# Performance work log

Hardware: AMD Instinct MI355X
Metric: run time of the kernel (lower is better)

Reference implementation:

```python
import jax, jax.numpy as jnp
import numpy as np

N = 262144
HID = 200


def _lin_init(k, out_d, in_d):
    k1, k2 = jax.random.split(k)
    bound = 1.0 / np.sqrt(in_d)
    W = jax.random.uniform(k1, (out_d, in_d), minval=-bound, maxval=bound, dtype=jnp.float32)
    b = jax.random.uniform(k2, (out_d,), minval=-bound, maxval=bound, dtype=jnp.float32)
    return W, b


def setup_inputs() -> dict:
    key = jax.random.key(0)
    ks = jax.random.split(key, 10)
    Wu0, bu0 = _lin_init(ks[0], HID, 3)
    Wu1, bu1 = _lin_init(ks[1], HID, HID)
    Wu2, bu2 = _lin_init(ks[2], 1, HID)
    Wv0, bv0 = _lin_init(ks[3], HID, 3)
    Wv1, bv1 = _lin_init(ks[4], HID, HID)
    Wv2, bv2 = _lin_init(ks[5], 1, HID)
    Wf0, bf0 = _lin_init(ks[6], HID, 12)
    Wf1, bf1 = _lin_init(ks[7], HID, HID)
    Wf2, bf2 = _lin_init(ks[8], 2, HID)
    inputs = jax.random.normal(ks[9], (N, 3), dtype=jnp.float32)
    return dict(inputs=inputs,
                Wu0=Wu0, bu0=bu0, Wu1=Wu1, bu1=bu1, Wu2=Wu2, bu2=bu2,
                Wv0=Wv0, bv0=bv0, Wv1=Wv1, bv1=bv1, Wv2=Wv2, bv2=bv2,
                Wf0=Wf0, bf0=bf0, Wf1=Wf1, bf1=bf1, Wf2=Wf2, bf2=bf2)


def _mlp(x, W0, b0, W1, b1, W2, b2):
    # NN with num_layers=3: sin(Linear) -> sin(Linear) -> Linear
    h = jnp.sin(x @ W0.T + b0)
    h = jnp.sin(h @ W1.T + b1)
    return h @ W2.T + b2


def _scalar(pt, params):
    # per-point scalar network, pt: [3]
    W0, b0, W1, b1, W2, b2 = params
    h = jnp.sin(W0 @ pt + b0)
    h = jnp.sin(W1 @ h + b1)
    return (W2 @ h + b2)[0]


def _derivs(pt, params):
    # first derivatives (grad) and diagonal second derivatives u_xx, u_yy
    # via forward-over-reverse (jvp of grad) with unit tangents e_x, e_y.
    g = jax.grad(lambda p: _scalar(p, params))
    ex = jnp.array([1.0, 0.0, 0.0], dtype=pt.dtype)
    ey = jnp.array([0.0, 1.0, 0.0], dtype=pt.dtype)
    grad, hx = jax.jvp(g, (pt,), (ex,))
    _, hy = jax.jvp(g, (pt,), (ey,))
    return grad, hx[0], hy[1]


def _dhpm_forward(inputs, pu, pv, pf):
    u = _mlp(inputs, *pu)  # [N,1]
    v = _mlp(inputs, *pv)  # [N,1]
    gu, u_xx, u_yy = jax.vmap(lambda p: _derivs(p, pu))(inputs)
    gv, v_xx, v_yy = jax.vmap(lambda p: _derivs(p, pv))(inputs)
    u_x, u_y, u_t = gu[:, :1], gu[:, 1:2], gu[:, 2:3]
    v_x, v_y, v_t = gv[:, :1], gv[:, 1:2], gv[:, 2:3]
    u_xx = u_xx[:, None]; u_yy = u_yy[:, None]
    v_xx = v_xx[:, None]; v_yy = v_yy[:, None]
    feat = jnp.concatenate([u, v, u_t, v_t, u_x, u_xx, u_y, u_yy,
                            v_x, v_xx, v_y, v_yy], axis=1)  # [N,12]
    f = _mlp(feat, *pf)  # [N,2]
    return (u, v, u_t, v_t, u_x, u_xx, u_y, u_yy,
            v_x, v_xx, v_y, v_yy, f[:, :1], f[:, 1:])


def reference(inputs, Wu0, bu0, Wu1, bu1, Wu2, bu2,
              Wv0, bv0, Wv1, bv1, Wv2, bv2,
              Wf0, bf0, Wf1, bf1, Wf2, bf2):
    pu = (Wu0, bu0, Wu1, bu1, Wu2, bu2)
    pv = (Wv0, bv0, Wv1, bv1, Wv2, bv2)
    pf = (Wf0, bf0, Wf1, bf1, Wf2, bf2)
    return _dhpm_forward(inputs, pu, pv, pf)
```

## Files before the change

kernel.cpp:

```cpp
#include <hip/hip_runtime.h>


#define HID 200
#define NPTS 128
#define NTHREADS 512
#define NT 13
#define KT 7
#define BLDK 232
#define BCHUNK 45056
#define FCHUNK 8192
#define XLDP 132

#define OFF_U  0
#define OFF_V  585728
#define OFF_F  1171456
#define OFF_CU 1277952
#define OFF_CV 1281152
#define OFF_CF 1284352

typedef _Float16 f16;
typedef _Float16 f16x2 __attribute__((ext_vector_type(2)));
typedef _Float16 f16x8 __attribute__((ext_vector_type(8)));
typedef float f32x4 __attribute__((ext_vector_type(4)));

#define GLDS16(gp, lp) __builtin_amdgcn_global_load_lds( \
    (const __attribute__((address_space(1))) void*)(gp), \
    (__attribute__((address_space(3))) void*)(lp), 16, 0, 0)

__global__ __launch_bounds__(256) void dhpm_prep(
    const float* __restrict__ Wu0, const float* __restrict__ bu0, const float* __restrict__ Wu1,
    const float* __restrict__ Wv0, const float* __restrict__ bv0, const float* __restrict__ Wv1,
    const float* __restrict__ Wf0, const float* __restrict__ bf0, const float* __restrict__ Wf1,
    char* __restrict__ ws)
{
    const int id = blockIdx.x * blockDim.x + threadIdx.x;
    const int nB = 2 * NT * 96 * 116;
    const int nF = NT * 16 * 116;
    if (id < nB) {
        int e = id;
        const int net = e / (NT*96*116); e -= net * (NT*96*116);
        const int nt  = e / (96*116);    e -= nt * (96*116);
        const int row = e / 116;
        const int k2  = e - row*116;
        const int ch  = row >> 4;
        const int j   = nt*16 + (row & 15);
        const int k   = k2*2;
        const float* W0 = net ? Wv0 : Wu0;
        const float* W1 = net ? Wv1 : Wu1;
        f16x2 v; v[0] = (f16)0.f; v[1] = (f16)0.f;
        if (j < HID) {
            #pragma unroll
            for (int s = 0; s < 2; ++s) {
                const int ks = k + s;
                if (ks < HID) {
                    const float w1 = W1[j*HID + ks];
                    const float ax = W0[ks*3+0], ay = W0[ks*3+1], at = W0[ks*3+2];
                    float gg;
                    if      (ch == 0) gg = 1.f;
                    else if (ch == 1) gg = -ax*ax;
                    else if (ch == 2) gg = -ay*ay;
                    else if (ch == 3) gg = ax;
                    else if (ch == 4) gg = ay;
                    else              gg = at;
                    v[s] = (f16)(w1 * gg);
                }
            }
        }
        *(f16x2*)(ws + (net ? OFF_V : OFF_U) + nt*BCHUNK + row*464 + k2*4) = v;
        return;
    }
    if (id < nB + nF) {
        int e = id - nB;
        const int nt  = e / (16*116);  e -= nt * (16*116);
        const int row = e / 116;
        const int k2  = e - row*116;
        const int j   = nt*16 + row;
        const int k   = k2*2;
        f16x2 v; v[0] = (f16)0.f; v[1] = (f16)0.f;
        if (j < HID) {
            if (k     < HID) v[0] = (f16)Wf1[j*HID + k];
            if (k + 1 < HID) v[1] = (f16)Wf1[j*HID + k + 1];
        }
        *(f16x2*)(ws + OFF_F + nt*FCHUNK + row*464 + k2*4) = v;
        return;
    }
    if (id < nB + nF + 400) {
        const int e = id - nB - nF;
        const int net = e / HID;
        const int r   = e - net*HID;
        const float* W0 = net ? Wv0 : Wu0;
        const float* b0 = net ? bv0 : bu0;
        float4 c;
        c.x = W0[r*3+0]; c.y = W0[r*3+1]; c.z = W0[r*3+2]; c.w = b0[r];
        *(float4*)(ws + (net ? OFF_CV : OFF_CU) + r*16) = c;
        return;
    }
    if (id < nB + nF + 400 + HID) {
        const int i = id - nB - nF - 400;
        float4 c0, c1, c2, c3;
        c0.x = Wf0[i*12+0];  c0.y = Wf0[i*12+1];  c0.z = Wf0[i*12+2];  c0.w = Wf0[i*12+3];
        c1.x = Wf0[i*12+4];  c1.y = Wf0[i*12+5];  c1.z = Wf0[i*12+6];  c1.w = Wf0[i*12+7];
        c2.x = Wf0[i*12+8];  c2.y = Wf0[i*12+9];  c2.z = Wf0[i*12+10]; c2.w = Wf0[i*12+11];
        c3.x = bf0[i]; c3.y = 0.f; c3.z = 0.f; c3.w = 0.f;
        char* p = ws + OFF_CF + i*64;
        *(float4*)(p)      = c0;
        *(float4*)(p + 16) = c1;
        *(float4*)(p + 32) = c2;
        *(float4*)(p + 48) = c3;
    }
}

__device__ __forceinline__ void run_net(
    const float* __restrict__ inp, const char* __restrict__ ws,
    const int cstOff, const int bOff,
    const float* __restrict__ b1, const float* __restrict__ W2, const float b2s,
    const int colV, const int colX, const int colXX,
    const int colY, const int colYY, const int colT,
    char* __restrict__ Bst, float* __restrict__ exch, float* __restrict__ featL,
    float* __restrict__ out, const int Np, const int gp0)
{
    const int t = threadIdx.x;
    const int lane = t & 63;
    const int w = __builtin_amdgcn_readfirstlane(t >> 6);
    const int q = w & 3, g = w >> 2;
    const int jl = lane & 15, klo = lane >> 4;

    const char* bsrc = ws + bOff;

    for (int c = w; c < 44; c += 8)
        GLDS16(bsrc + c*1024 + lane*16, Bst + c*1024);

    f16x8 afrag[2][KT];
    {
        const float4* cst = (const float4*)(ws + cstOff);
        #pragma unroll
        for (int mt = 0; mt < 2; ++mt) {
            const int prow = q*32 + mt*16 + jl;
            const float px = inp[(gp0+prow)*3+0];
            const float py = inp[(gp0+prow)*3+1];
            const float pz = inp[(gp0+prow)*3+2];
            #pragma unroll
            for (int kt = 0; kt < KT; ++kt) {
                f16x8 f;
                #pragma unroll
                for (int e = 0; e < 8; ++e) {
                    const int i = kt*32 + klo*8 + e;
                    const float4 c = cst[(i < HID) ? i : 0];
                    const float z = fmaf(c.x, px, fmaf(c.y, py, fmaf(c.z, pz, c.w)));
                    float sv;
                    if (g == 0) sv = __sinf(z); else sv = __cosf(z);
                    f[e] = (f16)sv;
                }
                afrag[mt][kt] = f;
            }
        }
    }

    float pA[2][4] = {{0,0,0,0},{0,0,0,0}};
    float pB[2][4] = {{0,0,0,0},{0,0,0,0}};
    float pC[2][4] = {{0,0,0,0},{0,0,0,0}};

    __syncthreads();

    for (int nt = 0; nt < NT; ++nt) {
        f32x4 acc[3][2];
        #pragma unroll
        for (int cc = 0; cc < 3; ++cc)
            #pragma unroll
            for (int mt = 0; mt < 2; ++mt) {
                f32x4 z = {0.f, 0.f, 0.f, 0.f};
                acc[cc][mt] = z;
            }
        const f16* BH = (const f16*)Bst;
        #pragma unroll
        for (int kt = 0; kt < KT; ++kt) {
            #pragma unroll
            for (int cc = 0; cc < 3; ++cc) {
                const f16x8 bfr = *(const f16x8*)&BH[((g*3+cc)*16 + jl)*BLDK + kt*32 + klo*8];
                acc[cc][0] = __builtin_amdgcn_mfma_f32_16x16x32_f16(afrag[0][kt], bfr, acc[cc][0], 0,0,0);
                acc[cc][1] = __builtin_amdgcn_mfma_f32_16x16x32_f16(afrag[1][kt], bfr, acc[cc][1], 0,0,0);
            }
        }

        #pragma unroll
        for (int mt = 0; mt < 2; ++mt) {
            const int pt0 = q*32 + mt*16 + klo*4;
            if (g == 0) {
                *(f32x4*)&exch[(0*16 + jl)*XLDP + pt0] = acc[0][mt];
            } else {
                *(f32x4*)&exch[(1*16 + jl)*XLDP + pt0] = acc[0][mt];
                *(f32x4*)&exch[(2*16 + jl)*XLDP + pt0] = acc[1][mt];
            }
        }
        __syncthreads();

        if (nt + 1 < NT) {
            const char* src = bsrc + (nt+1)*BCHUNK;
            for (int c = w; c < 44; c += 8)
                GLDS16(src + c*1024 + lane*16, Bst + c*1024);
        }

        const int j = nt*16 + jl;
        const float b1j = (j < HID) ? b1[j] : 0.f;
        const float w2j = (j < HID) ? W2[j] : 0.f;
        #pragma unroll
        for (int mt = 0; mt < 2; ++mt) {
            const int pt0 = q*32 + mt*16 + klo*4;
            if (g == 0) {
                const f32x4 yx = *(const f32x4*)&exch[(1*16 + jl)*XLDP + pt0];
                const f32x4 yy = *(const f32x4*)&exch[(2*16 + jl)*XLDP + pt0];
                #pragma unroll
                for (int r = 0; r < 4; ++r) {
                    float s1, c1;
                    __sincosf(acc[0][mt][r] + b1j, &s1, &c1);
                    const float wc = w2j*c1, wsn = w2j*s1;
                    pA[mt][r] += wsn;
                    pB[mt][r] = fmaf(wc, acc[1][mt][r], fmaf(-wsn*yx[r], yx[r], pB[mt][r]));
                    pC[mt][r] = fmaf(wc, acc[2][mt][r], fmaf(-wsn*yy[r], yy[r], pC[mt][r]));
                }
            } else {
                const f32x4 y0 = *(const f32x4*)&exch[(0*16 + jl)*XLDP + pt0];
                #pragma unroll
                for (int r = 0; r < 4; ++r) {
                    float s1, c1;
                    __sincosf(y0[r] + b1j, &s1, &c1);
                    const float wc = w2j*c1;
                    pA[mt][r] = fmaf(wc, acc[0][mt][r], pA[mt][r]);
                    pB[mt][r] = fmaf(wc, acc[1][mt][r], pB[mt][r]);
                    pC[mt][r] = fmaf(wc, acc[2][mt][r], pC[mt][r]);
                }
            }
        }
        __syncthreads();
    }

    #pragma unroll
    for (int d = 1; d < 16; d <<= 1) {
        #pragma unroll
        for (int mt = 0; mt < 2; ++mt)
            #pragma unroll
            for (int r = 0; r < 4; ++r) {
                pA[mt][r] += __shfl_xor(pA[mt][r], d);
                pB[mt][r] += __shfl_xor(pB[mt][r], d);
                pC[mt][r] += __shfl_xor(pC[mt][r], d);
            }
    }
    if (jl == 0) {
        #pragma unroll
        for (int mt = 0; mt < 2; ++mt) {
            const int pt0 = q*32 + mt*16 + klo*4;
            f32x4 vA, vB, vC;
            #pragma unroll
            for (int r = 0; r < 4; ++r) {
                vA[r] = pA[mt][r] + ((g == 0) ? b2s : 0.f);
                vB[r] = pB[mt][r];
                vC[r] = pC[mt][r];
            }
            const int cA = (g == 0) ? colV  : colX;
            const int cB = (g == 0) ? colXX : colY;
            const int cC = (g == 0) ? colYY : colT;
            *(f32x4*)&out[(size_t)cA*Np + gp0 + pt0] = vA;
            *(f32x4*)&out[(size_t)cB*Np + gp0 + pt0] = vB;
            *(f32x4*)&out[(size_t)cC*Np + gp0 + pt0] = vC;
            #pragma unroll
            for (int r = 0; r < 4; ++r) {
                featL[(pt0+r)*13 + cA] = vA[r];
                featL[(pt0+r)*13 + cB] = vB[r];
                featL[(pt0+r)*13 + cC] = vC[r];
            }
        }
    }
}

__global__ __launch_bounds__(NTHREADS) void dhpm_main(
    const float* __restrict__ inp, const char* __restrict__ ws,
    const float* __restrict__ bu1, const float* __restrict__ Wu2, const float* __restrict__ bu2,
    const float* __restrict__ bv1, const float* __restrict__ Wv2, const float* __restrict__ bv2,
    const float* __restrict__ bf1, const float* __restrict__ Wf2, const float* __restrict__ bf2,
    float* __restrict__ out, const int Np)
{
    __shared__ __align__(16) char Bst[BCHUNK];
    __shared__ __align__(16) float exch[3*16*XLDP];
    __shared__ float featL[NPTS*13];

    const int t = threadIdx.x;
    const int lane = t & 63;
    const int w = __builtin_amdgcn_readfirstlane(t >> 6);
    const int jl = lane & 15, klo = lane >> 4;
    const int gp0 = blockIdx.x * NPTS;

    run_net(inp, ws, OFF_CU, OFF_U, bu1, Wu2, bu2[0], 0, 4, 5, 6, 7, 2,
            Bst, (float*)exch, featL, out, Np, gp0);
    run_net(inp, ws, OFF_CV, OFF_V, bv1, Wv2, bv2[0], 1, 8, 9, 10, 11, 3,
            Bst, (float*)exch, featL, out, Np, gp0);

    GLDS16(ws + OFF_F + w*1024 + lane*16, Bst + w*1024);
    __syncthreads();

    f16x8 affrag[KT];
    {
        const float4* cf = (const float4*)(ws + OFF_CF);
        const int prow = w*16 + jl;
        float fv[12];
        #pragma unroll
        for (int k = 0; k < 12; ++k) fv[k] = featL[prow*13 + k];
        #pragma unroll
        for (int kt = 0; kt < KT; ++kt) {
            f16x8 f;
            #pragma unroll
            for (int e = 0; e < 8; ++e) {
                const int i = kt*32 + klo*8 + e;
                const int ic = (i < HID) ? i : 0;
                const float4 c0 = cf[ic*4+0];
                const float4 c1 = cf[ic*4+1];
                const float4 c2 = cf[ic*4+2];
                const float4 c3 = cf[ic*4+3];
                float z = c3.x;
                z = fmaf(c0.x, fv[0], z);  z = fmaf(c0.y, fv[1], z);
                z = fmaf(c0.z, fv[2], z);  z = fmaf(c0.w, fv[3], z);
                z = fmaf(c1.x, fv[4], z);  z = fmaf(c1.y, fv[5], z);
                z = fmaf(c1.z, fv[6], z);  z = fmaf(c1.w, fv[7], z);
                z = fmaf(c2.x, fv[8], z);  z = fmaf(c2.y, fv[9], z);
                z = fmaf(c2.z, fv[10], z); z = fmaf(c2.w, fv[11], z);
                f[e] = (f16)__sinf(z);
            }
            affrag[kt] = f;
        }
    }

    float pf0[4] = {0,0,0,0}, pf1[4] = {0,0,0,0};
    for (int nt = 0; nt < NT; ++nt) {
        f32x4 acc = {0.f, 0.f, 0.f, 0.f};
        const f16* F = (const f16*)Bst;
        #pragma unroll
        for (int kt = 0; kt < KT; ++kt) {
            const f16x8 bfr = *(const f16x8*)&F[jl*BLDK + kt*32 + klo*8];
            acc = __builtin_amdgcn_mfma_f32_16x16x32_f16(affrag[kt], bfr, acc, 0,0,0);
        }
        __syncthreads();
        if (nt + 1 < NT)
            GLDS16(ws + OFF_F + (nt+1)*FCHUNK + w*1024 + lane*16, Bst + w*1024);
        const int j = nt*16 + jl;
        const float bj = (j < HID) ? bf1[j] : 0.f;
        const float wa = (j < HID) ? Wf2[j] : 0.f;
        const float wb = (j < HID) ? Wf2[HID + j] : 0.f;
        #pragma unroll
        for (int r = 0; r < 4; ++r) {
            const float h = __sinf(acc[r] + bj);
            pf0[r] = fmaf(wa, h, pf0[r]);
            pf1[r] = fmaf(wb, h, pf1[r]);
        }
        __syncthreads();
    }

    #pragma unroll
    for (int d = 1; d < 16; d <<= 1)
        #pragma unroll
        for (int r = 0; r < 4; ++r) {
            pf0[r] += __shfl_xor(pf0[r], d);
            pf1[r] += __shfl_xor(pf1[r], d);
        }
    if (jl == 0) {
        const int pt0 = w*16 + klo*4;
        f32x4 v0, v1;
        #pragma unroll
        for (int r = 0; r < 4; ++r) {
            v0[r] = pf0[r] + bf2[0];
            v1[r] = pf1[r] + bf2[1];
        }
        *(f32x4*)&out[(size_t)12*Np + gp0 + pt0] = v0;
        *(f32x4*)&out[(size_t)13*Np + gp0 + pt0] = v1;
    }
}

extern "C" void kernel_launch(void* const* d_in, const int* in_sizes, int n_in,
                              void* d_out, int out_size, void* d_ws, size_t ws_size,
                              hipStream_t stream) {
    const float* inp = (const float*)d_in[0];
    const float* Wu0 = (const float*)d_in[1];  const float* bu0 = (const float*)d_in[2];
    const float* Wu1 = (const float*)d_in[3];  const float* bu1 = (const float*)d_in[4];
    const float* Wu2 = (const float*)d_in[5];  const float* bu2 = (const float*)d_in[6];
    const float* Wv0 = (const float*)d_in[7];  const float* bv0 = (const float*)d_in[8];
    const float* Wv1 = (const float*)d_in[9];  const float* bv1 = (const float*)d_in[10];
    const float* Wv2 = (const float*)d_in[11]; const float* bv2 = (const float*)d_in[12];
    const float* Wf0 = (const float*)d_in[13]; const float* bf0 = (const float*)d_in[14];
    const float* Wf1 = (const float*)d_in[15]; const float* bf1 = (const float*)d_in[16];
    const float* Wf2 = (const float*)d_in[17]; const float* bf2 = (const float*)d_in[18];
    float* out = (float*)d_out;
    char* ws = (char*)d_ws;

    const int Np = in_sizes[0] / 3;

    const int nTot = 2*NT*96*116 + NT*16*116 + 400 + HID;
    dhpm_prep<<<(nTot + 255) / 256, 256, 0, stream>>>(
        Wu0, bu0, Wu1, Wv0, bv0, Wv1, Wf0, bf0, Wf1, ws);
    dhpm_main<<<Np / NPTS, NTHREADS, 0, stream>>>(
        inp, ws, bu1, Wu2, bu2, bv1, Wv2, bv2, bf1, Wf2, bf2, out, Np);
}
```

Baseline: 648.3 us.

## Give each wave all six tangent columns and double-buffer weight chunks

Each wave now handles 32 points and computes both the sin and cos tangent A-fragments, so all six B-column groups are processed per wave. This removes the cross-wave LDS exchange and its extra barrier per tile, and doubles the points per block to 256. Weight chunks are double-buffered in LDS so the next tile's global-to-LDS load overlaps the current MFMAs. Outputs are staged in LDS and written coalesced at the end. The cost is a much higher register count (two A-fragment sets and 12 accumulators) and larger LDS use, which may limit occupancy despite the launch bound of 2.

New measurement: 1.017 ms. 56.8% more time.

```diff
diff --git a/kernel.cpp b/kernel.cpp
--- a/kernel.cpp
+++ b/kernel.cpp
@@ -2,14 +2,13 @@
 
 
 #define HID 200
-#define NPTS 128
+#define NPTS 256
 #define NTHREADS 512
 #define NT 13
 #define KT 7
 #define BLDK 232
 #define BCHUNK 45056
 #define FCHUNK 8192
-#define XLDP 132
 
 #define OFF_U  0
 #define OFF_V  585728
@@ -110,266 +109,295 @@
     }
 }
 
+__device__ __forceinline__ f32x4 mfma16(f16x8 a, f16x8 b, f32x4 c) {
+    return __builtin_amdgcn_mfma_f32_16x16x32_f16(a, b, c, 0, 0, 0);
+}
+
 __device__ __forceinline__ void run_net(
     const float* __restrict__ inp, const char* __restrict__ ws,
     const int cstOff, const int bOff,
     const float* __restrict__ b1, const float* __restrict__ W2, const float b2s,
-    const int colV, const int colX, const int colXX,
-    const int colY, const int colYY, const int colT,
-    char* __restrict__ Bst, float* __restrict__ exch, float* __restrict__ featL,
-    float* __restrict__ out, const int Np, const int gp0)
+    const int cV, const int cXX, const int cYY,
+    const int cX, const int cY, const int cT,
+    char* __restrict__ Bb0, char* __restrict__ Bb1, float* __restrict__ res,
+    const int gp0)
 {
     const int t = threadIdx.x;
     const int lane = t & 63;
     const int w = __builtin_amdgcn_readfirstlane(t >> 6);
-    const int q = w & 3, g = w >> 2;
     const int jl = lane & 15, klo = lane >> 4;
-
+    const int o = w * 32;
     const char* bsrc = ws + bOff;
 
     for (int c = w; c < 44; c += 8)
-        GLDS16(bsrc + c*1024 + lane*16, Bst + c*1024);
-
-    f16x8 afrag[2][KT];
+        GLDS16(bsrc + c*1024 + lane*16, Bb0 + c*1024);
+
+    f16x8 aS[2][KT], aC[2][KT];
     {
         const float4* cst = (const float4*)(ws + cstOff);
         #pragma unroll
         for (int mt = 0; mt < 2; ++mt) {
-            const int prow = q*32 + mt*16 + jl;
-            const float px = inp[(gp0+prow)*3+0];
-            const float py = inp[(gp0+prow)*3+1];
-            const float pz = inp[(gp0+prow)*3+2];
+            const int prow = gp0 + o + mt*16 + jl;
+            const float x = inp[prow*3+0], y = inp[prow*3+1], tt = inp[prow*3+2];
             #pragma unroll
             for (int kt = 0; kt < KT; ++kt) {
-                f16x8 f;
+                f16x8 fs, fc;
                 #pragma unroll
                 for (int e = 0; e < 8; ++e) {
                     const int i = kt*32 + klo*8 + e;
                     const float4 c = cst[(i < HID) ? i : 0];
-                    const float z = fmaf(c.x, px, fmaf(c.y, py, fmaf(c.z, pz, c.w)));
-                    float sv;
-                    if (g == 0) sv = __sinf(z); else sv = __cosf(z);
-                    f[e] = (f16)sv;
+                    const float z = fmaf(c.x, x, fmaf(c.y, y, fmaf(c.z, tt, c.w)));
+                    float sv, cv;
+                    __sincosf(z, &sv, &cv);
+                    fs[e] = (f16)sv; fc[e] = (f16)cv;
                 }
-                afrag[mt][kt] = f;
-            }
-        }
-    }
-
-    float pA[2][4] = {{0,0,0,0},{0,0,0,0}};
-    float pB[2][4] = {{0,0,0,0},{0,0,0,0}};
-    float pC[2][4] = {{0,0,0,0},{0,0,0,0}};
+                aS[mt][kt] = fs; aC[mt][kt] = fc;
+            }
+        }
+    }
+
+    float pV[2][4], pXX[2][4], pYY[2][4], pX[2][4], pY[2][4], pT[2][4];
+    #pragma unroll
+    for (int mt = 0; mt < 2; ++mt)
+        #pragma unroll
+        for (int r = 0; r < 4; ++r) {
+            pV[mt][r]=0.f; pXX[mt][r]=0.f; pYY[mt][r]=0.f;
+            pX[mt][r]=0.f; pY[mt][r]=0.f; pT[mt][r]=0.f;
+        }
 
     __syncthreads();
 
-    for (int nt = 0; nt < NT; ++nt) {
-        f32x4 acc[3][2];
-        #pragma unroll
-        for (int cc = 0; cc < 3; ++cc)
+    auto step = [&](const char* Bcur, char* Bnext, const int nt, const int ntNext) {
+        if (ntNext < NT)
+            for (int c = w; c < 44; c += 8)
+                GLDS16(bsrc + ntNext*BCHUNK + c*1024 + lane*16, Bnext + c*1024);
+
+        const f16* BH = (const f16*)Bcur;
+        f32x4 acc[6][2];
+        #pragma unroll
+        for (int c = 0; c < 6; ++c)
             #pragma unroll
             for (int mt = 0; mt < 2; ++mt) {
-                f32x4 z = {0.f, 0.f, 0.f, 0.f};
-                acc[cc][mt] = z;
-            }
-        const f16* BH = (const f16*)Bst;
+                f32x4 z = {0.f,0.f,0.f,0.f};
+                acc[c][mt] = z;
+            }
         #pragma unroll
         for (int kt = 0; kt < KT; ++kt) {
-            #pragma unroll
-            for (int cc = 0; cc < 3; ++cc) {
-                const f16x8 bfr = *(const f16x8*)&BH[((g*3+cc)*16 + jl)*BLDK + kt*32 + klo*8];
-                acc[cc][0] = __builtin_amdgcn_mfma_f32_16x16x32_f16(afrag[0][kt], bfr, acc[cc][0], 0,0,0);
-                acc[cc][1] = __builtin_amdgcn_mfma_f32_16x16x32_f16(afrag[1][kt], bfr, acc[cc][1], 0,0,0);
-            }
-        }
-
-        #pragma unroll
-        for (int mt = 0; mt < 2; ++mt) {
-            const int pt0 = q*32 + mt*16 + klo*4;
-            if (g == 0) {
-                *(f32x4*)&exch[(0*16 + jl)*XLDP + pt0] = acc[0][mt];
-            } else {
-                *(f32x4*)&exch[(1*16 + jl)*XLDP + pt0] = acc[0][mt];
-                *(f32x4*)&exch[(2*16 + jl)*XLDP + pt0] = acc[1][mt];
-            }
-        }
-        __syncthreads();
-
-        if (nt + 1 < NT) {
-            const char* src = bsrc + (nt+1)*BCHUNK;
-            for (int c = w; c < 44; c += 8)
-                GLDS16(src + c*1024 + lane*16, Bst + c*1024);
+            f16x8 bfr[6];
+            #pragma unroll
+            for (int c = 0; c < 6; ++c)
+                bfr[c] = *(const f16x8*)&BH[(c*16 + jl)*BLDK + kt*32 + klo*8];
+            #pragma unroll
+            for (int c = 0; c < 3; ++c) {
+                acc[c][0] = mfma16(aS[0][kt], bfr[c], acc[c][0]);
+                acc[c][1] = mfma16(aS[1][kt], bfr[c], acc[c][1]);
+            }
+            #pragma unroll
+            for (int c = 3; c < 6; ++c) {
+                acc[c][0] = mfma16(aC[0][kt], bfr[c], acc[c][0]);
+                acc[c][1] = mfma16(aC[1][kt], bfr[c], acc[c][1]);
+            }
         }
 
         const int j = nt*16 + jl;
         const float b1j = (j < HID) ? b1[j] : 0.f;
         const float w2j = (j < HID) ? W2[j] : 0.f;
         #pragma unroll
+        for (int mt = 0; mt < 2; ++mt)
+            #pragma unroll
+            for (int r = 0; r < 4; ++r) {
+                float s1, c1;
+                __sincosf(acc[0][mt][r] + b1j, &s1, &c1);
+                const float wc = w2j*c1, wsn = w2j*s1;
+                const float ydx = acc[3][mt][r], ydy = acc[4][mt][r];
+                pV[mt][r]  += wsn;
+                pXX[mt][r] = fmaf(wc, acc[1][mt][r], fmaf(-wsn*ydx, ydx, pXX[mt][r]));
+                pYY[mt][r] = fmaf(wc, acc[2][mt][r], fmaf(-wsn*ydy, ydy, pYY[mt][r]));
+                pX[mt][r]  = fmaf(wc, ydx, pX[mt][r]);
+                pY[mt][r]  = fmaf(wc, ydy, pY[mt][r]);
+                pT[mt][r]  = fmaf(wc, acc[5][mt][r], pT[mt][r]);
+            }
+        __syncthreads();
+    };
+
+    #pragma unroll
+    for (int ntp = 0; ntp < 6; ++ntp) {
+        step(Bb0, Bb1, ntp*2,     ntp*2 + 1);
+        step(Bb1, Bb0, ntp*2 + 1, ntp*2 + 2);
+    }
+    step(Bb0, Bb1, 12, NT);
+
+    #pragma unroll
+    for (int d = 1; d < 16; d <<= 1)
+        #pragma unroll
+        for (int mt = 0; mt < 2; ++mt)
+            #pragma unroll
+            for (int r = 0; r < 4; ++r) {
+                pV[mt][r]  += __shfl_xor(pV[mt][r],  d);
+                pXX[mt][r] += __shfl_xor(pXX[mt][r], d);
+                pYY[mt][r] += __shfl_xor(pYY[mt][r], d);
+                pX[mt][r]  += __shfl_xor(pX[mt][r],  d);
+                pY[mt][r]  += __shfl_xor(pY[mt][r],  d);
+                pT[mt][r]  += __shfl_xor(pT[mt][r],  d);
+            }
+    if (jl == 0) {
+        #pragma unroll
         for (int mt = 0; mt < 2; ++mt) {
-            const int pt0 = q*32 + mt*16 + klo*4;
-            if (g == 0) {
-                const f32x4 yx = *(const f32x4*)&exch[(1*16 + jl)*XLDP + pt0];
-                const f32x4 yy = *(const f32x4*)&exch[(2*16 + jl)*XLDP + pt0];
-                #pragma unroll
-                for (int r = 0; r < 4; ++r) {
-                    float s1, c1;
-                    __sincosf(acc[0][mt][r] + b1j, &s1, &c1);
-                    const float wc = w2j*c1, wsn = w2j*s1;
-                    pA[mt][r] += wsn;
-                    pB[mt][r] = fmaf(wc, acc[1][mt][r], fmaf(-wsn*yx[r], yx[r], pB[mt][r]));
-                    pC[mt][r] = fmaf(wc, acc[2][mt][r], fmaf(-wsn*yy[r], yy[r], pC[mt][r]));
-                }
-            } else {
-                const f32x4 y0 = *(const f32x4*)&exch[(0*16 + jl)*XLDP + pt0];
-                #pragma unroll
-                for (int r = 0; r < 4; ++r) {
-                    float s1, c1;
-                    __sincosf(y0[r] + b1j, &s1, &c1);
-                    const float wc = w2j*c1;
-                    pA[mt][r] = fmaf(wc, acc[0][mt][r], pA[mt][r]);
-                    pB[mt][r] = fmaf(wc, acc[1][mt][r], pB[mt][r]);
-                    pC[mt][r] = fmaf(wc, acc[2][mt][r], pC[mt][r]);
-                }
-            }
-        }
-        __syncthreads();
-    }
-
-    #pragma unroll
-    for (int d = 1; d < 16; d <<= 1) {
-        #pragma unroll
-        for (int mt = 0; mt < 2; ++mt)
-            #pragma unroll
-            for (int r = 0; r < 4; ++r) {
-                pA[mt][r] += __shfl_xor(pA[mt][r], d);
-                pB[mt][r] += __shfl_xor(pB[mt][r], d);
-                pC[mt][r] += __shfl_xor(pC[mt][r], d);
-            }
-    }
-    if (jl == 0) {
-        #pragma unroll
-        for (int mt = 0; mt < 2; ++mt) {
-            const int pt0 = q*32 + mt*16 + klo*4;
-            f32x4 vA, vB, vC;
-            #pragma unroll
-            for (int r = 0; r < 4; ++r) {
-                vA[r] = pA[mt][r] + ((g == 0) ? b2s : 0.f);
-                vB[r] = pB[mt][r];
-                vC[r] = pC[mt][r];
-            }
-            const int cA = (g == 0) ? colV  : colX;
-            const int cB = (g == 0) ? colXX : colY;
-            const int cC = (g == 0) ? colYY : colT;
-            *(f32x4*)&out[(size_t)cA*Np + gp0 + pt0] = vA;
-            *(f32x4*)&out[(size_t)cB*Np + gp0 + pt0] = vB;
-            *(f32x4*)&out[(size_t)cC*Np + gp0 + pt0] = vC;
-            #pragma unroll
-            for (int r = 0; r < 4; ++r) {
-                featL[(pt0+r)*13 + cA] = vA[r];
-                featL[(pt0+r)*13 + cB] = vB[r];
-                featL[(pt0+r)*13 + cC] = vC[r];
-            }
+            const int p0 = o + mt*16 + klo*4;
+            f32x4 vv;
+            #pragma unroll
+            for (int r = 0; r < 4; ++r) vv[r] = pV[mt][r] + b2s;
+            *(f32x4*)&res[cV*264 + p0] = vv;
+            #pragma unroll
+            for (int r = 0; r < 4; ++r) vv[r] = pXX[mt][r];
+            *(f32x4*)&res[cXX*264 + p0] = vv;
+            #pragma unroll
+            for (int r = 0; r < 4; ++r) vv[r] = pYY[mt][r];
+            *(f32x4*)&res[cYY*264 + p0] = vv;
+            #pragma unroll
+            for (int r = 0; r < 4; ++r) vv[r] = pX[mt][r];
+            *(f32x4*)&res[cX*264 + p0] = vv;
+            #pragma unroll
+            for (int r = 0; r < 4; ++r) vv[r] = pY[mt][r];
+            *(f32x4*)&res[cY*264 + p0] = vv;
+            #pragma unroll
+            for (int r = 0; r < 4; ++r) vv[r] = pT[mt][r];
+            *(f32x4*)&res[cT*264 + p0] = vv;
         }
     }
 }
 
-__global__ __launch_bounds__(NTHREADS) void dhpm_main(
+__global__ __launch_bounds__(NTHREADS, 2) void dhpm_main(
     const float* __restrict__ inp, const char* __restrict__ ws,
     const float* __restrict__ bu1, const float* __restrict__ Wu2, const float* __restrict__ bu2,
     const float* __restrict__ bv1, const float* __restrict__ Wv2, const float* __restrict__ bv2,
     const float* __restrict__ bf1, const float* __restrict__ Wf2, const float* __restrict__ bf2,
     float* __restrict__ out, const int Np)
 {
-    __shared__ __align__(16) char Bst[BCHUNK];
-    __shared__ __align__(16) float exch[3*16*XLDP];
-    __shared__ float featL[NPTS*13];
+    __shared__ __align__(16) char Bb0[BCHUNK];
+    __shared__ __align__(16) char Bb1[BCHUNK];
+    __shared__ __align__(16) float res[14*264];
 
     const int t = threadIdx.x;
     const int lane = t & 63;
     const int w = __builtin_amdgcn_readfirstlane(t >> 6);
     const int jl = lane & 15, klo = lane >> 4;
+    const int o = w * 32;
     const int gp0 = blockIdx.x * NPTS;
 
-    run_net(inp, ws, OFF_CU, OFF_U, bu1, Wu2, bu2[0], 0, 4, 5, 6, 7, 2,
-            Bst, (float*)exch, featL, out, Np, gp0);
-    run_net(inp, ws, OFF_CV, OFF_V, bv1, Wv2, bv2[0], 1, 8, 9, 10, 11, 3,
-            Bst, (float*)exch, featL, out, Np, gp0);
-
-    GLDS16(ws + OFF_F + w*1024 + lane*16, Bst + w*1024);
+    run_net(inp, ws, OFF_CU, OFF_U, bu1, Wu2, bu2[0], 0, 5, 7, 4, 6, 2,
+            Bb0, Bb1, res, gp0);
+    run_net(inp, ws, OFF_CV, OFF_V, bv1, Wv2, bv2[0], 1, 9, 11, 8, 10, 3,
+            Bb0, Bb1, res, gp0);
+
+    for (int c = w; c < 8; c += 8)
+        GLDS16(ws + OFF_F + c*1024 + lane*16, Bb0 + c*1024);
     __syncthreads();
 
-    f16x8 affrag[KT];
+    f16x8 aF[2][KT];
     {
         const float4* cf = (const float4*)(ws + OFF_CF);
-        const int prow = w*16 + jl;
-        float fv[12];
-        #pragma unroll
-        for (int k = 0; k < 12; ++k) fv[k] = featL[prow*13 + k];
+        #pragma unroll
+        for (int mt = 0; mt < 2; ++mt) {
+            const int p = o + mt*16 + jl;
+            float fv[12];
+            #pragma unroll
+            for (int k = 0; k < 12; ++k) fv[k] = res[k*264 + p];
+            #pragma unroll
+            for (int kt = 0; kt < KT; ++kt) {
+                f16x8 f;
+                #pragma unroll
+                for (int e = 0; e < 8; ++e) {
+                    const int i = kt*32 + klo*8 + e;
+                    const int ic = (i < HID) ? i : 0;
+                    const float4 c0 = cf[ic*4+0];
+                    const float4 c1 = cf[ic*4+1];
+                    const float4 c2 = cf[ic*4+2];
+                    const float4 c3 = cf[ic*4+3];
+                    float z = c3.x;
+                    z = fmaf(c0.x, fv[0], z);  z = fmaf(c0.y, fv[1], z);
+                    z = fmaf(c0.z, fv[2], z);  z = fmaf(c0.w, fv[3], z);
+                    z = fmaf(c1.x, fv[4], z);  z = fmaf(c1.y, fv[5], z);
+                    z = fmaf(c1.z, fv[6], z);  z = fmaf(c1.w, fv[7], z);
+                    z = fmaf(c2.x, fv[8], z);  z = fmaf(c2.y, fv[9], z);
+                    z = fmaf(c2.z, fv[10], z); z = fmaf(c2.w, fv[11], z);
+                    f[e] = (f16)__sinf(z);
+                }
+                aF[mt][kt] = f;
+            }
+        }
+    }
+
+    float pf0[2][4], pf1[2][4];
+    #pragma unroll
+    for (int mt = 0; mt < 2; ++mt)
+        #pragma unroll
+        for (int r = 0; r < 4; ++r) { pf0[mt][r] = 0.f; pf1[mt][r] = 0.f; }
+
+    auto fstep = [&](const char* Bcur, char* Bnext, const int nt, const int ntNext) {
+        if (ntNext < NT)
+            for (int c = w; c < 8; c += 8)
+                GLDS16(ws + OFF_F + ntNext*FCHUNK + c*1024 + lane*16, Bnext + c*1024);
+        const f16* BH = (const f16*)Bcur;
+        f32x4 acc[2];
+        #pragma unroll
+        for (int mt = 0; mt < 2; ++mt) { f32x4 z = {0.f,0.f,0.f,0.f}; acc[mt] = z; }
         #pragma unroll
         for (int kt = 0; kt < KT; ++kt) {
-            f16x8 f;
-            #pragma unroll
-            for (int e = 0; e < 8; ++e) {
-                const int i = kt*32 + klo*8 + e;
-                const int ic = (i < HID) ? i : 0;
-                const float4 c0 = cf[ic*4+0];
-                const float4 c1 = cf[ic*4+1];
-                const float4 c2 = cf[ic*4+2];
-                const float4 c3 = cf[ic*4+3];
-                float z = c3.x;
-                z = fmaf(c0.x, fv[0], z);  z = fmaf(c0.y, fv[1], z);
-                z = fmaf(c0.z, fv[2], z);  z = fmaf(c0.w, fv[3], z);
-                z = fmaf(c1.x, fv[4], z);  z = fmaf(c1.y, fv[5], z);
-                z = fmaf(c1.z, fv[6], z);  z = fmaf(c1.w, fv[7], z);
-                z = fmaf(c2.x, fv[8], z);  z = fmaf(c2.y, fv[9], z);
-                z = fmaf(c2.z, fv[10], z); z = fmaf(c2.w, fv[11], z);
-                f[e] = (f16)__sinf(z);
-            }
-            affrag[kt] = f;
-        }
-    }
-
-    float pf0[4] = {0,0,0,0}, pf1[4] = {0,0,0,0};
-    for (int nt = 0; nt < NT; ++nt) {
-        f32x4 acc = {0.f, 0.f, 0.f, 0.f};
-        const f16* F = (const f16*)Bst;
-        #pragma unroll
-        for (int kt = 0; kt < KT; ++kt) {
-            const f16x8 bfr = *(const f16x8*)&F[jl*BLDK + kt*32 + klo*8];
-            acc = __builtin_amdgcn_mfma_f32_16x16x32_f16(affrag[kt], bfr, acc, 0,0,0);
-        }
-        __syncthreads();
-        if (nt + 1 < NT)
-            GLDS16(ws + OFF_F + (nt+1)*FCHUNK + w*1024 + lane*16, Bst + w*1024);
+            const f16x8 bfr = *(const f16x8*)&BH[jl*BLDK + kt*32 + klo*8];
+            acc[0] = mfma16(aF[0][kt], bfr, acc[0]);
+            acc[1] = mfma16(aF[1][kt], bfr, acc[1]);
+        }
         const int j = nt*16 + jl;
         const float bj = (j < HID) ? bf1[j] : 0.f;
         const float wa = (j < HID) ? Wf2[j] : 0.f;
         const float wb = (j < HID) ? Wf2[HID + j] : 0.f;
         #pragma unroll
-        for (int r = 0; r < 4; ++r) {
-            const float h = __sinf(acc[r] + bj);
-            pf0[r] = fmaf(wa, h, pf0[r]);
-            pf1[r] = fmaf(wb, h, pf1[r]);
-        }
+        for (int mt = 0; mt < 2; ++mt)
+            #pragma unroll
+            for (int r = 0; r < 4; ++r) {
+                const float h = __sinf(acc[mt][r] + bj);
+                pf0[mt][r] = fmaf(wa, h, pf0[mt][r]);
+                pf1[mt][r] = fmaf(wb, h, pf1[mt][r]);
+            }
         __syncthreads();
-    }
+    };
+
+    #pragma unroll
+    for (int ntp = 0; ntp < 6; ++ntp) {
+        fstep(Bb0, Bb1, ntp*2,     ntp*2 + 1);
+        fstep(Bb1, Bb0, ntp*2 + 1, ntp*2 + 2);
+    }
+    fstep(Bb0, Bb1, 12, NT);
 
     #pragma unroll
     for (int d = 1; d < 16; d <<= 1)
         #pragma unroll
-        for (int r = 0; r < 4; ++r) {
-            pf0[r] += __shfl_xor(pf0[r], d);
-            pf1[r] += __shfl_xor(pf1[r], d);
-        }
+        for (int mt = 0; mt < 2; ++mt)
+            #pragma unroll
+            for (int r = 0; r < 4; ++r) {
+                pf0[mt][r] += __shfl_xor(pf0[mt][r], d);
+                pf1[mt][r] += __shfl_xor(pf1[mt][r], d);
+            }
     if (jl == 0) {
-        const int pt0 = w*16 + klo*4;
-        f32x4 v0, v1;
-        #pragma unroll
-        for (int r = 0; r < 4; ++r) {
-            v0[r] = pf0[r] + bf2[0];
-            v1[r] = pf1[r] + bf2[1];
-        }
-        *(f32x4*)&out[(size_t)12*Np + gp0 + pt0] = v0;
-        *(f32x4*)&out[(size_t)13*Np + gp0 + pt0] = v1;
+        #pragma unroll
+        for (int mt = 0; mt < 2; ++mt) {
+            const int p0 = o + mt*16 + klo*4;
+            f32x4 v0, v1;
+            #pragma unroll
+            for (int r = 0; r < 4; ++r) {
+                v0[r] = pf0[mt][r] + bf2[0];
+                v1[r] = pf1[mt][r] + bf2[1];
+            }
+            *(f32x4*)&res[12*264 + p0] = v0;
+            *(f32x4*)&res[13*264 + p0] = v1;
+        }
+    }
+    __syncthreads();
+
+    for (int e = t; e < 14*256; e += NTHREADS) {
+        const int c = e >> 8, p = e & 255;
+        out[(size_t)c*Np + gp0 + p] = res[c*264 + p];
     }
 }
 
```
